# Performance work log

Measured on AMD Instinct MI355X. Metric: run time of the kernel, lower is better.

The kernel has to match this reference:

```python
import jax, jax.numpy as jnp
import numpy as np

BOHR = 0.5291772105638411   # Angstrom per Bohr (ase.units.Bohr)
HA = 27.211386024367243     # eV per Hartree (ase.units.Ha)
S6, S8, A1, A2 = 1.0, 0.7875, 0.4289, 4.4407
CN_ONSET, CN_CUTOFF = 20.0, 25.0
E2_ONSET, E2_CUTOFF = 55.0, 60.0
KCN = 16.0   # exponent of ncoord.exp_count
WF = 4.0     # gaussian_weight factor

N_ATOMS = 100000
N_EDGES = 3200000
N_ELEM = 95
N_REF = 5


def smooth_cutoff(dr, r_onset, r_cutoff):
    """HOOMD-style C^1 multiplicative isotropic cutoff S(dr)."""
    r_c = jnp.float32(r_cutoff) ** jnp.float32(2)
    r_o = jnp.float32(r_onset) ** jnp.float32(2)
    r = dr ** jnp.float32(2)
    inner = jnp.where(
        dr < r_cutoff,
        (r_c - r) ** 2 * (r_c + 2 * r - 3 * r_o) / (r_c - r_o) ** 3,
        0.0,
    )
    return jnp.where(dr < r_onset, 1.0, inner)


def setup_inputs() -> dict:
    key = jax.random.key(0)
    k1, k2, k3, k4, k5, k6, k7 = jax.random.split(key, 7)
    dr_vec = jax.random.normal(k1, (N_EDGES, 3), dtype=jnp.float32)
    ref_cn_table = jax.random.uniform(k2, (N_ELEM, N_REF), dtype=jnp.float32)
    ref_c6_table = jax.random.uniform(k3, (N_ELEM, N_ELEM, N_REF, N_REF), dtype=jnp.float32)
    r4r2_table = jax.random.uniform(k4, (N_ELEM,), dtype=jnp.float32) + 0.5
    rcov_table = jax.random.uniform(k5, (N_ELEM,), dtype=jnp.float32) + 0.5
    numbers = jax.random.randint(k6, (N_ATOMS,), 0, N_ELEM, dtype=jnp.int32)
    idx = jax.random.randint(k7, (2, N_EDGES), 0, N_ATOMS, dtype=jnp.int32)
    return {
        "dr_vec": dr_vec,
        "ref_cn_table": ref_cn_table,
        "ref_c6_table": ref_c6_table,
        "r4r2_table": r4r2_table,
        "rcov_table": rcov_table,
        "numbers": numbers,
        "idx": idx,
    }


def reference(dr_vec, ref_cn_table, ref_c6_table, r4r2_table, rcov_table, numbers, idx):
    n_atoms = numbers.shape[0]
    # per-edge distance, Angstrom -> Bohr
    dr = jnp.sqrt(jnp.sum(dr_vec * dr_vec, axis=-1)) / jnp.float32(BOHR)  # [E]
    i, j = idx[0], idx[1]
    Zi, Zj = numbers[i], numbers[j]

    # per-edge element data (D3Data.from_idxs)
    rc = rcov_table[Zi] + rcov_table[Zj]            # [E]
    qq = 3.0 * r4r2_table[Zi] * r4r2_table[Zj]      # [E]

    # coordination numbers: exp_count with smooth cutoff, segment-summed per atom
    count = 1.0 / (1.0 + jnp.exp(-KCN * (rc / dr - 1.0)))
    masked_cn = jnp.where(dr > 0, smooth_cutoff(dr, CN_ONSET, CN_CUTOFF) * count, 0.0)
    cn = jax.ops.segment_sum(masked_cn, i, num_segments=n_atoms)  # [N]

    # reference weights (gaussian weighting, normalized)
    ref_cn = ref_cn_table[numbers]                  # [N, R]
    dcn = ref_cn - cn[:, None]
    w = jnp.where(ref_cn >= 0, jnp.exp(-WF * dcn * dcn), 0.0)
    weights = w / (jnp.sum(w, -1, keepdims=True) + jnp.finfo(cn.dtype).eps)  # [N, R]

    # atomic C6 per edge
    ref_c6 = ref_c6_table[Zj, Zi]                   # [E, R, R]
    gw2 = weights[i][:, None, :] * weights[j][:, :, None]  # [E, R, R]
    c6 = jnp.sum(gw2 * ref_c6, axis=(-1, -2))       # [E]

    # rational (Becke-Johnson) damped two-body dispersion energy
    rr = A1 * jnp.sqrt(qq) + A2
    dr2 = dr * dr
    dr6 = dr2 * dr2 * dr2
    dr8 = dr6 * dr2
    rr2 = rr * rr
    rr6 = rr2 * rr2 * rr2
    rr8 = rr6 * rr2
    damped = -c6 * (S6 / (dr6 + rr6) + S8 * qq / (dr8 + rr8))
    energy = smooth_cutoff(dr, E2_ONSET, E2_CUTOFF) * damped / 2.0
    return jnp.sum(energy) * jnp.float32(HA)
```

## Files before the change

kernel.cpp:

```cpp
#include <hip/hip_runtime.h>
#include <hip/hip_fp16.h>

#define BOHR_F 0.5291772105638411f
#define HA_D   27.211386024367243
#define A1_F   0.4289f
#define A2_F   4.4407f
#define S6_F   1.0f
#define S8_F   0.7875f
#define KCN_F  16.0f
#define WF_F   4.0f
#define EPS_F  1.1920929e-07f

#define Q15_SCALE 32767.0f
#define Q15_INV   (1.0f/32767.0f)
#define DR_SCALE  512.0f
#define DR_INV    (1.0f/512.0f)
#define CN_SCALE 8388608.0f
#define CN_INV   (1.0f/8388608.0f)

#define NELEM  95
#define C6PADH 32
#define NBLK   512
#define BSW    512

__device__ __forceinline__ float smooth_cutoff(float dr, float r_on, float r_cut) {
    float r_c = r_cut * r_cut;
    float r_o = r_on * r_on;
    float r   = dr * dr;
    float den = (r_c - r_o);
    float t   = r_c - r;
    float inner = (dr < r_cut)
        ? (t * t * (r_c + 2.0f * r - 3.0f * r_o)) / (den * den * den)
        : 0.0f;
    return (dr < r_on) ? 1.0f : inner;
}

__device__ __forceinline__ float edge_m(float dr, float rc) {
    if (!(dr > 0.0f)) return 0.0f;
    float count = 1.0f / (1.0f + expf(-KCN_F * (rc / dr - 1.0f)));
    return smooth_cutoff(dr, 20.0f, 25.0f) * count;
}

__device__ __forceinline__ void u2f2(unsigned u, float& a, float& b) {
    __half2 h = __builtin_bit_cast(__half2, u);
    float2 f = __half22float2(h);
    a = f.x; b = f.y;
}

__device__ __forceinline__ int zfromR(uint4 R) {
    float z, dum;
    u2f2(R.w, z, dum);
    return (int)z;
}

__device__ __forceinline__ float edge_e(float dr, uint4 Ri, uint4 Rj,
                                        uint4 c0, uint4 c1, uint4 c2, uint4 c3) {
    float wi[5], wj[5], qi, qj;
    u2f2(Ri.x, wi[0], wi[1]); u2f2(Ri.y, wi[2], wi[3]); u2f2(Ri.z, wi[4], qi);
    u2f2(Rj.x, wj[0], wj[1]); u2f2(Rj.y, wj[2], wj[3]); u2f2(Rj.z, wj[4], qj);
    float ct[26];
    u2f2(c0.x, ct[0],  ct[1]);  u2f2(c0.y, ct[2],  ct[3]);
    u2f2(c0.z, ct[4],  ct[5]);  u2f2(c0.w, ct[6],  ct[7]);
    u2f2(c1.x, ct[8],  ct[9]);  u2f2(c1.y, ct[10], ct[11]);
    u2f2(c1.z, ct[12], ct[13]); u2f2(c1.w, ct[14], ct[15]);
    u2f2(c2.x, ct[16], ct[17]); u2f2(c2.y, ct[18], ct[19]);
    u2f2(c2.z, ct[20], ct[21]); u2f2(c2.w, ct[22], ct[23]);
    u2f2(c3.x, ct[24], ct[25]);
    float c6 = 0.0f;
#pragma unroll
    for (int a = 0; a < 5; ++a)
#pragma unroll
        for (int b = 0; b < 5; ++b)
            c6 += wj[a] * wi[b] * ct[a * 5 + b];
    float qq = 3.0f * qi * qj;
    float rr = A1_F * sqrtf(qq) + A2_F;
    float dr2 = dr * dr;
    float dr6 = dr2 * dr2 * dr2;
    float dr8 = dr6 * dr2;
    float rr2 = rr * rr;
    float rr6 = rr2 * rr2 * rr2;
    float rr8 = rr6 * rr2;
    float damped = -c6 * (S6_F / (dr6 + rr6) + S8_F * qq / (dr8 + rr8));
    return smooth_cutoff(dr, 55.0f, 60.0f) * damped * 0.5f;
}

__global__ __launch_bounds__(256)
void k_prep_c6(const float* __restrict__ src, __half* __restrict__ dst, int ntot) {
    int o = blockIdx.x * blockDim.x + threadIdx.x;
    if (o >= ntot) return;
    int p = o >> 5;
    int t = o & 31;
    dst[o] = __float2half((t < 25) ? src[p * 25 + t] : 0.0f);
}

__global__ __launch_bounds__(256)
void k_prep_atom(const int* __restrict__ numbers, const float* __restrict__ rcov,
                 uint2* __restrict__ rcovZ, int n_atoms) {
    int a = blockIdx.x * blockDim.x + threadIdx.x;
    if (a >= n_atoms) return;
    int Z = numbers[a];
    rcovZ[a] = make_uint2(__float_as_uint(rcov[Z]), (unsigned)Z);
}

__global__ __launch_bounds__(BSW, 4)
void k_bin(const float* __restrict__ dr_vec,
           const int* __restrict__ idx_i, const int* __restrict__ idx_j,
           const uint2* __restrict__ rcovZ,
           unsigned* __restrict__ packed2,
           unsigned* __restrict__ ghist,
           int n_edges, int nb) {
    __shared__ unsigned hist[256];
    if (threadIdx.x < 256) hist[threadIdx.x] = 0;
    __syncthreads();
    int nquad = (n_edges + 3) >> 2;
    int stride = gridDim.x * blockDim.x;
    for (int qd = blockIdx.x * blockDim.x + threadIdx.x; qd < nquad; qd += stride) {
        int e0 = qd << 2;
        int ne = n_edges - e0; if (ne > 4) ne = 4;
        if (ne == 4) {
            float4 v0 = *reinterpret_cast<const float4*>(dr_vec + 3 * e0);
            float4 v1 = *reinterpret_cast<const float4*>(dr_vec + 3 * e0 + 4);
            float4 v2 = *reinterpret_cast<const float4*>(dr_vec + 3 * e0 + 8);
            float drq[4];
            drq[0] = sqrtf(v0.x*v0.x + v0.y*v0.y + v0.z*v0.z) / BOHR_F;
            drq[1] = sqrtf(v0.w*v0.w + v1.x*v1.x + v1.y*v1.y) / BOHR_F;
            drq[2] = sqrtf(v1.z*v1.z + v1.w*v1.w + v2.x*v2.x) / BOHR_F;
            drq[3] = sqrtf(v2.y*v2.y + v2.z*v2.z + v2.w*v2.w) / BOHR_F;
            int4 i4 = *reinterpret_cast<const int4*>(idx_i + e0);
            int4 j4 = *reinterpret_cast<const int4*>(idx_j + e0);
            int ia[4] = { i4.x, i4.y, i4.z, i4.w };
            int ja[4] = { j4.x, j4.y, j4.z, j4.w };
            uint2 RiZ[4], RjZ[4];
#pragma unroll
            for (int k = 0; k < 4; ++k) { RiZ[k] = rcovZ[ia[k]]; RjZ[k] = rcovZ[ja[k]]; }
            unsigned w0[4], w1[4];
#pragma unroll
            for (int k = 0; k < 4; ++k) {
                float rc = __uint_as_float(RiZ[k].x) + __uint_as_float(RjZ[k].x);
                float m = edge_m(drq[k], rc);
                unsigned q = (unsigned)(m * Q15_SCALE + 0.5f);
                if (q > 0x7FFFu) q = 0x7FFFu;
                unsigned dq = (unsigned)(drq[k] * DR_SCALE + 0.5f);
                if (dq > 0x7FFFu) dq = 0x7FFFu;
                w0[k] = ((unsigned)ia[k] << 15) | q;
                w1[k] = ((unsigned)ja[k] << 15) | dq;
                atomicAdd(&hist[ia[k] >> 9], 1u);
            }
            *reinterpret_cast<uint4*>(packed2 + 2 * e0) =
                make_uint4(w0[0], w1[0], w0[1], w1[1]);
            *reinterpret_cast<uint4*>(packed2 + 2 * e0 + 4) =
                make_uint4(w0[2], w1[2], w0[3], w1[3]);
        } else {
            for (int k = 0; k < ne; ++k) {
                int e = e0 + k;
                float x = dr_vec[3*e], y = dr_vec[3*e+1], z = dr_vec[3*e+2];
                float dr = sqrtf(x*x + y*y + z*z) / BOHR_F;
                int i = idx_i[e], j = idx_j[e];
                uint2 RiZ = rcovZ[i], RjZ = rcovZ[j];
                float m = edge_m(dr, __uint_as_float(RiZ.x) + __uint_as_float(RjZ.x));
                unsigned q = (unsigned)(m * Q15_SCALE + 0.5f);
                if (q > 0x7FFFu) q = 0x7FFFu;
                unsigned dq = (unsigned)(dr * DR_SCALE + 0.5f);
                if (dq > 0x7FFFu) dq = 0x7FFFu;
                packed2[2*e]   = ((unsigned)i << 15) | q;
                packed2[2*e+1] = ((unsigned)j << 15) | dq;
                atomicAdd(&hist[i >> 9], 1u);
            }
        }
    }
    __syncthreads();
    if ((int)threadIdx.x < nb)
        ghist[(size_t)threadIdx.x * gridDim.x + blockIdx.x] = hist[threadIdx.x];
}

__global__ __launch_bounds__(NBLK)
void k_scan_bucket(unsigned* __restrict__ ghist, unsigned* __restrict__ totals) {
    __shared__ unsigned s[NBLK];
    int b = blockIdx.x;
    int t = threadIdx.x;
    unsigned v = ghist[(size_t)b * NBLK + t];
    s[t] = v;
    __syncthreads();
    for (int off = 1; off < NBLK; off <<= 1) {
        unsigned x = (t >= off) ? s[t - off] : 0u;
        __syncthreads();
        s[t] += x;
        __syncthreads();
    }
    ghist[(size_t)b * NBLK + t] = s[t] - v;
    if (t == NBLK - 1) totals[b] = s[t];
}

__global__ __launch_bounds__(256)
void k_scan_base(const unsigned* __restrict__ totals,
                 unsigned* __restrict__ base, int nb) {
    __shared__ unsigned s[256];
    int t = threadIdx.x;
    unsigned v = (t < nb) ? totals[t] : 0u;
    s[t] = v;
    __syncthreads();
    for (int off = 1; off < 256; off <<= 1) {
        unsigned x = (t >= off) ? s[t - off] : 0u;
        __syncthreads();
        s[t] += x;
        __syncthreads();
    }
    if (t < nb) base[t] = s[t] - v;
    if (t == 255) base[nb] = s[t];
}

__global__ __launch_bounds__(BSW, 4)
void k_scatter(const unsigned* __restrict__ packed2,
               const unsigned* __restrict__ ghist,
               const unsigned* __restrict__ base,
               uint2* __restrict__ pairs,
               int n_edges, int nb) {
    __shared__ unsigned ofs[256];
    if ((int)threadIdx.x < nb)
        ofs[threadIdx.x] = base[threadIdx.x]
                         + ghist[(size_t)threadIdx.x * gridDim.x + blockIdx.x];
    __syncthreads();
    int nquad = (n_edges + 3) >> 2;
    int stride = gridDim.x * blockDim.x;
    for (int qd = blockIdx.x * blockDim.x + threadIdx.x; qd < nquad; qd += stride) {
        int e0 = qd << 2;
        int ne = n_edges - e0; if (ne > 4) ne = 4;
        if (ne == 4) {
            uint4 pA = *reinterpret_cast<const uint4*>(packed2 + 2 * e0);
            uint4 pB = *reinterpret_cast<const uint4*>(packed2 + 2 * e0 + 4);
            unsigned w0[4] = { pA.x, pA.z, pB.x, pB.z };
            unsigned w1[4] = { pA.y, pA.w, pB.y, pB.w };
#pragma unroll
            for (int k = 0; k < 4; ++k) {
                unsigned pos = atomicAdd(&ofs[w0[k] >> 24], 1u);
                pairs[pos] = make_uint2(w0[k], w1[k]);
            }
        } else {
            for (int k = 0; k < ne; ++k) {
                int e = e0 + k;
                unsigned w0 = packed2[2*e], w1 = packed2[2*e+1];
                unsigned pos = atomicAdd(&ofs[w0 >> 24], 1u);
                pairs[pos] = make_uint2(w0, w1);
            }
        }
    }
}

__global__ __launch_bounds__(512)
void k_reduce_weights(const uint2* __restrict__ pairs,
                      const unsigned* __restrict__ base,
                      const int* __restrict__ numbers,
                      const float* __restrict__ ref_cn_table,
                      const float* __restrict__ r4r2,
                      __half* __restrict__ rec,
                      int n_atoms) {
    __shared__ unsigned hist[512];
    hist[threadIdx.x] = 0;
    __syncthreads();
    int b = blockIdx.x;
    unsigned start = base[b];
    unsigned end   = base[b + 1];
    for (unsigned k = start + threadIdx.x; k < end; k += 512) {
        unsigned p = pairs[k].x;
        atomicAdd(&hist[(p >> 15) & 511], p & 0x7FFFu);
    }
    __syncthreads();
    int a = (b << 9) + threadIdx.x;
    if (a < n_atoms) {
        float c = (float)hist[threadIdx.x] * Q15_INV;
        int Z = numbers[a];
        float w[5];
        float s = 0.0f;
#pragma unroll
        for (int r = 0; r < 5; ++r) {
            float rcn = ref_cn_table[Z * 5 + r];
            float d = rcn - c;
            float wv = (rcn >= 0.0f) ? expf(-WF_F * d * d) : 0.0f;
            w[r] = wv;
            s += wv;
        }
        float den = s + EPS_F;
        __half* rr = rec + (size_t)a * 8;
#pragma unroll
        for (int r = 0; r < 5; ++r) rr[r] = __float2half(w[r] / den);
        rr[5] = __float2half(r4r2[Z]);
        rr[6] = __float2half((float)Z);
        rr[7] = __float2half(0.0f);
    }
}

#define LOADC(p, z) do { \
    const uint4* _cp = reinterpret_cast<const uint4*>(c6h + (size_t)(z) * C6PADH); \
    p##0 = _cp[0]; p##1 = _cp[1]; p##2 = _cp[2]; p##3 = _cp[3]; } while (0)

__global__ __launch_bounds__(256, 1)
void k_energy_sorted(const uint2* __restrict__ pairs,
                     const __half* __restrict__ rec,
                     const __half* __restrict__ c6h,
                     double* __restrict__ e_acc,
                     int n_edges) {
    double local = 0.0;
    const uint4* recv = reinterpret_cast<const uint4*>(rec);
    int nquad = n_edges >> 2;
    int tid = blockIdx.x * blockDim.x + threadIdx.x;
    int stride = gridDim.x * blockDim.x;
    for (int qd = tid; qd < nquad; qd += stride) {
        int e0 = qd << 2;
        uint4 pA = *reinterpret_cast<const uint4*>(pairs + e0);
        uint4 pB = *reinterpret_cast<const uint4*>(pairs + e0 + 2);
        unsigned i0 = pA.x >> 15, j0 = pA.y >> 15;
        unsigned i1 = pA.z >> 15, j1 = pA.w >> 15;
        unsigned i2 = pB.x >> 15, j2 = pB.y >> 15;
        unsigned i3 = pB.z >> 15, j3 = pB.w >> 15;
        float dr0 = (float)(pA.y & 0x7FFFu) * DR_INV;
        float dr1 = (float)(pA.w & 0x7FFFu) * DR_INV;
        float dr2 = (float)(pB.y & 0x7FFFu) * DR_INV;
        float dr3 = (float)(pB.w & 0x7FFFu) * DR_INV;
        uint4 Ri0 = recv[i0], Rj0 = recv[j0];
        uint4 Ri1 = recv[i1], Rj1 = recv[j1];
        uint4 Ri2 = recv[i2], Rj2 = recv[j2];
        uint4 Ri3 = recv[i3], Rj3 = recv[j3];
        int zp0 = zfromR(Rj0) * NELEM + zfromR(Ri0);
        int zp1 = zfromR(Rj1) * NELEM + zfromR(Ri1);
        int zp2 = zfromR(Rj2) * NELEM + zfromR(Ri2);
        int zp3 = zfromR(Rj3) * NELEM + zfromR(Ri3);
        uint4 a0, a1, a2, a3;   LOADC(a, zp0);
        uint4 b0, b1, b2, b3;   LOADC(b, zp1);
        uint4 c0, c1, c2, c3;   LOADC(c, zp2);
        uint4 d0, d1, d2, d3;   LOADC(d, zp3);
        local += (double)edge_e(dr0, Ri0, Rj0, a0, a1, a2, a3);
        local += (double)edge_e(dr1, Ri1, Rj1, b0, b1, b2, b3);
        local += (double)edge_e(dr2, Ri2, Rj2, c0, c1, c2, c3);
        local += (double)edge_e(dr3, Ri3, Rj3, d0, d1, d2, d3);
    }
    for (int e = (nquad << 2) + tid; e < n_edges; e += stride) {
        uint2 pr = pairs[e];
        unsigned i = pr.x >> 15;
        unsigned j = pr.y >> 15;
        float dr = (float)(pr.y & 0x7FFFu) * DR_INV;
        uint4 Ri = recv[i];
        uint4 Rj = recv[j];
        int zp = zfromR(Rj) * NELEM + zfromR(Ri);
        const uint4* cp = reinterpret_cast<const uint4*>(c6h + (size_t)zp * C6PADH);
        local += (double)edge_e(dr, Ri, Rj, cp[0], cp[1], cp[2], cp[3]);
    }

    __shared__ double sdata[4];
    for (int off = 32; off > 0; off >>= 1)
        local += __shfl_down(local, off, 64);
    int lane = threadIdx.x & 63;
    int wid  = threadIdx.x >> 6;
    if (lane == 0) sdata[wid] = local;
    __syncthreads();
    if (threadIdx.x == 0) {
        double s = sdata[0] + sdata[1] + sdata[2] + sdata[3];
        atomicAdd(e_acc, s);
    }
}

__global__ __launch_bounds__(256)
void k_edges_cn_atomic(const float* __restrict__ dr_vec,
                       const int* __restrict__ idx_i,
                       const int* __restrict__ idx_j,
                       const uint2* __restrict__ rcovZ,
                       unsigned* __restrict__ cn_u32,
                       int n_edges) {
    int e = blockIdx.x * blockDim.x + threadIdx.x;
    if (e >= n_edges) return;
    float x = dr_vec[3 * e + 0];
    float y = dr_vec[3 * e + 1];
    float z = dr_vec[3 * e + 2];
    float dr = sqrtf(x * x + y * y + z * z) / BOHR_F;
    int i = idx_i[e];
    int j = idx_j[e];
    uint2 RiZ = rcovZ[i], RjZ = rcovZ[j];
    float m = edge_m(dr, __uint_as_float(RiZ.x) + __uint_as_float(RjZ.x));
    unsigned q = (unsigned)(m * CN_SCALE + 0.5f);
    if (q) atomicAdd(&cn_u32[i], q);
}

__global__ __launch_bounds__(256)
void k_atom_weights_rec(const unsigned* __restrict__ cn_u32,
                        const int* __restrict__ numbers,
                        const float* __restrict__ ref_cn_table,
                        const float* __restrict__ r4r2,
                        __half* __restrict__ rec,
                        int n_atoms) {
    int a = blockIdx.x * blockDim.x + threadIdx.x;
    if (a >= n_atoms) return;
    float c = (float)cn_u32[a] * CN_INV;
    int Z = numbers[a];
    float w[5];
    float s = 0.0f;
#pragma unroll
    for (int r = 0; r < 5; ++r) {
        float rcn = ref_cn_table[Z * 5 + r];
        float d = rcn - c;
        float wv = (rcn >= 0.0f) ? expf(-WF_F * d * d) : 0.0f;
        w[r] = wv;
        s += wv;
    }
    float den = s + EPS_F;
    __half* rr = rec + (size_t)a * 8;
#pragma unroll
    for (int r = 0; r < 5; ++r) rr[r] = __float2half(w[r] / den);
    rr[5] = __float2half(r4r2[Z]);
    rr[6] = __float2half((float)Z);
    rr[7] = __float2half(0.0f);
}

__global__ __launch_bounds__(256)
void k_energy_unsorted(const float* __restrict__ dr_vec,
                       const int* __restrict__ idx_i,
                       const int* __restrict__ idx_j,
                       const __half* __restrict__ rec,
                       const __half* __restrict__ c6h,
                       double* __restrict__ e_acc,
                       int n_edges) {
    double local = 0.0;
    const uint4* recv = reinterpret_cast<const uint4*>(rec);
    int tid = blockIdx.x * blockDim.x + threadIdx.x;
    int stride = gridDim.x * blockDim.x;
    for (int e = tid; e < n_edges; e += stride) {
        float x = dr_vec[3*e], y = dr_vec[3*e+1], z = dr_vec[3*e+2];
        float dr = sqrtf(x*x + y*y + z*z) / BOHR_F;
        int i = idx_i[e], j = idx_j[e];
        uint4 Ri = recv[i];
        uint4 Rj = recv[j];
        int zp = zfromR(Rj) * NELEM + zfromR(Ri);
        const uint4* cp = reinterpret_cast<const uint4*>(c6h + (size_t)zp * C6PADH);
        local += (double)edge_e(dr, Ri, Rj, cp[0], cp[1], cp[2], cp[3]);
    }
    __shared__ double sdata[4];
    for (int off = 32; off > 0; off >>= 1)
        local += __shfl_down(local, off, 64);
    int lane = threadIdx.x & 63;
    int wid  = threadIdx.x >> 6;
    if (lane == 0) sdata[wid] = local;
    __syncthreads();
    if (threadIdx.x == 0) {
        double s = sdata[0] + sdata[1] + sdata[2] + sdata[3];
        atomicAdd(e_acc, s);
    }
}

__global__ void k_finalize(const double* __restrict__ e_acc,
                           float* __restrict__ out) {
    out[0] = (float)(e_acc[0] * HA_D);
}

static inline size_t a16(size_t x) { return (x + 15) & ~(size_t)15; }

extern "C" void kernel_launch(void* const* d_in, const int* in_sizes, int n_in,
                              void* d_out, int out_size, void* d_ws, size_t ws_size,
                              hipStream_t stream) {
    const float* dr_vec      = (const float*)d_in[0];
    const float* ref_cn_tab  = (const float*)d_in[1];
    const float* ref_c6_tab  = (const float*)d_in[2];
    const float* r4r2        = (const float*)d_in[3];
    const float* rcov        = (const float*)d_in[4];
    const int*   numbers     = (const int*)d_in[5];
    const int*   idx         = (const int*)d_in[6];

    int n_atoms = in_sizes[5];
    int n_edges = in_sizes[6] / 2;
    const int* idx_i = idx;
    const int* idx_j = idx + n_edges;

    const int BS = 256;
    int nb = (n_atoms + 511) >> 9;
    int c6tot = NELEM * NELEM * C6PADH;

    char* ws = (char*)d_ws;
    double* e_acc = (double*)ws;

    size_t off_rec = 16;
    size_t off_c6p = a16(off_rec + (size_t)n_atoms * 8 * 2);
    size_t off_rcZ = a16(off_c6p + (size_t)c6tot * 2);
    size_t off_var = a16(off_rcZ + (size_t)n_atoms * 8);

    size_t s_packed = off_var;
    size_t s_pairs  = a16(s_packed + (size_t)n_edges * 8);
    size_t s_ghist  = a16(s_pairs + (size_t)n_edges * 8);
    size_t s_tot    = a16(s_ghist + (size_t)nb * NBLK * 4);
    size_t s_base   = a16(s_tot + (size_t)nb * 4);
    size_t need_s   = s_base + (size_t)(nb + 1) * 4;

    size_t a_cn   = off_var;

    int grid_c6 = (c6tot + BS - 1) / BS;
    int grid_a  = (n_atoms + BS - 1) / BS;
    int nquad   = (n_edges + 3) >> 2;
    int grid_q  = (nquad + BS - 1) / BS;
    if (grid_q > 8192) grid_q = 8192;
    int grid_e1 = (n_edges + BS - 1) / BS;
    if (grid_e1 > 8192) grid_e1 = 8192;

    __half* rec   = (__half*)(ws + off_rec);
    __half* c6h   = (__half*)(ws + off_c6p);
    uint2*  rcovZ = (uint2*)(ws + off_rcZ);

    k_prep_c6<<<grid_c6, BS, 0, stream>>>(ref_c6_tab, c6h, c6tot);
    k_prep_atom<<<grid_a, BS, 0, stream>>>(numbers, rcov, rcovZ, n_atoms);

    bool sortable = (n_atoms <= (1 << 17)) && (nb <= 256);

    if (sortable && ws_size >= need_s) {
        unsigned* packed2 = (unsigned*)(ws + s_packed);
        uint2*    pairs   = (uint2*)(ws + s_pairs);
        unsigned* ghist   = (unsigned*)(ws + s_ghist);
        unsigned* totals  = (unsigned*)(ws + s_tot);
        unsigned* base    = (unsigned*)(ws + s_base);

        hipMemsetAsync(d_ws, 0, 16, stream);

        k_bin<<<NBLK, BSW, 0, stream>>>(dr_vec, idx_i, idx_j, rcovZ,
            packed2, ghist, n_edges, nb);
        k_scan_bucket<<<nb, NBLK, 0, stream>>>(ghist, totals);
        k_scan_base<<<1, 256, 0, stream>>>(totals, base, nb);
        k_scatter<<<NBLK, BSW, 0, stream>>>(packed2, ghist, base, pairs,
                                            n_edges, nb);
        k_reduce_weights<<<nb, 512, 0, stream>>>(pairs, base, numbers,
            ref_cn_tab, r4r2, rec, n_atoms);
        k_energy_sorted<<<grid_q, BS, 0, stream>>>(pairs, rec, c6h, e_acc,
                                                   n_edges);
    } else {
        unsigned* cn_u32 = (unsigned*)(ws + a_cn);
        hipMemsetAsync(d_ws, 0, 16, stream);
        hipMemsetAsync(cn_u32, 0, (size_t)n_atoms * 4, stream);

        int grid_e = (n_edges + BS - 1) / BS;
        k_edges_cn_atomic<<<grid_e, BS, 0, stream>>>(dr_vec, idx_i, idx_j,
            rcovZ, cn_u32, n_edges);
        k_atom_weights_rec<<<grid_a, BS, 0, stream>>>(cn_u32, numbers,
            ref_cn_tab, r4r2, rec, n_atoms);
        k_energy_unsorted<<<grid_e1, BS, 0, stream>>>(dr_vec, idx_i, idx_j,
            rec, c6h, e_acc, n_edges);
    }

    k_finalize<<<1, 1, 0, stream>>>(e_acc, (float*)d_out);
}
```

Measured before the change: 157.7 us.

## Quantize C6 table to 8-bit rows and fuse edge compute into scatter

The per-pair C6 reference block is stored as 25 uint8 values plus a per-row float scale (32 bytes instead of 64), which halves the gather traffic in the energy kernel. The binning pass now only histograms idx_i, and the scatter pass recomputes distances and coordination terms directly from the inputs. This removes the intermediate packed buffer write and read. The cost is reading dr_vec, idx and rcovZ in the scatter instead, plus precision loss from 8-bit C6 quantization, which may break tolerance.

```diff
diff --git a/kernel.cpp b/kernel.cpp
--- a/kernel.cpp
+++ b/kernel.cpp
@@ -19,7 +19,6 @@
 #define CN_INV   (1.0f/8388608.0f)
 
 #define NELEM  95
-#define C6PADH 32
 #define NBLK   512
 #define BSW    512
 
@@ -53,25 +52,24 @@
     return (int)z;
 }
 
-__device__ __forceinline__ float edge_e(float dr, uint4 Ri, uint4 Rj,
-                                        uint4 c0, uint4 c1, uint4 c2, uint4 c3) {
+__device__ __forceinline__ float edge_e8(float dr, uint4 Ri, uint4 Rj,
+                                         uint4 c0, uint4 c1) {
     float wi[5], wj[5], qi, qj;
     u2f2(Ri.x, wi[0], wi[1]); u2f2(Ri.y, wi[2], wi[3]); u2f2(Ri.z, wi[4], qi);
     u2f2(Rj.x, wj[0], wj[1]); u2f2(Rj.y, wj[2], wj[3]); u2f2(Rj.z, wj[4], qj);
-    float ct[26];
-    u2f2(c0.x, ct[0],  ct[1]);  u2f2(c0.y, ct[2],  ct[3]);
-    u2f2(c0.z, ct[4],  ct[5]);  u2f2(c0.w, ct[6],  ct[7]);
-    u2f2(c1.x, ct[8],  ct[9]);  u2f2(c1.y, ct[10], ct[11]);
-    u2f2(c1.z, ct[12], ct[13]); u2f2(c1.w, ct[14], ct[15]);
-    u2f2(c2.x, ct[16], ct[17]); u2f2(c2.y, ct[18], ct[19]);
-    u2f2(c2.z, ct[20], ct[21]); u2f2(c2.w, ct[22], ct[23]);
-    u2f2(c3.x, ct[24], ct[25]);
-    float c6 = 0.0f;
-#pragma unroll
-    for (int a = 0; a < 5; ++a)
-#pragma unroll
-        for (int b = 0; b < 5; ++b)
-            c6 += wj[a] * wi[b] * ct[a * 5 + b];
+    unsigned w[7] = { c0.x, c0.y, c0.z, c0.w, c1.x, c1.y, c1.z };
+    float sc = __uint_as_float(c1.w);
+    float c6q = 0.0f;
+#pragma unroll
+    for (int a = 0; a < 5; ++a) {
+#pragma unroll
+        for (int b = 0; b < 5; ++b) {
+            const int k = a * 5 + b;
+            float qv = (float)((w[k >> 2] >> ((k & 3) * 8)) & 0xFFu);
+            c6q += wj[a] * wi[b] * qv;
+        }
+    }
+    float c6 = c6q * sc;
     float qq = 3.0f * qi * qj;
     float rr = A1_F * sqrtf(qq) + A2_F;
     float dr2 = dr * dr;
@@ -85,12 +83,38 @@
 }
 
 __global__ __launch_bounds__(256)
-void k_prep_c6(const float* __restrict__ src, __half* __restrict__ dst, int ntot) {
-    int o = blockIdx.x * blockDim.x + threadIdx.x;
-    if (o >= ntot) return;
-    int p = o >> 5;
-    int t = o & 31;
-    dst[o] = __float2half((t < 25) ? src[p * 25 + t] : 0.0f);
+void k_prep_c6u8(const float* __restrict__ src, unsigned char* __restrict__ dst,
+                 int nrows) {
+    int r = blockIdx.x * blockDim.x + threadIdx.x;
+    if (r >= nrows) return;
+    const float* s = src + (size_t)r * 25;
+    float mx = 0.0f;
+#pragma unroll
+    for (int k = 0; k < 25; ++k) mx = fmaxf(mx, fabsf(s[k]));
+    float sc  = mx * (1.0f / 255.0f);
+    float inv = (mx > 0.0f) ? 255.0f / mx : 0.0f;
+    unsigned w[8];
+#pragma unroll
+    for (int v = 0; v < 7; ++v) {
+        unsigned acc = 0;
+#pragma unroll
+        for (int b = 0; b < 4; ++b) {
+            int k = v * 4 + b;
+            unsigned q = 0;
+            if (k < 25) {
+                float t = s[k] * inv;
+                t = fmaxf(t, 0.0f);
+                q = (unsigned)(t + 0.5f);
+                if (q > 255u) q = 255u;
+            }
+            acc |= q << (b * 8);
+        }
+        w[v] = acc;
+    }
+    w[7] = __float_as_uint(sc);
+    uint4* d = reinterpret_cast<uint4*>(dst + (size_t)r * 32);
+    d[0] = make_uint4(w[0], w[1], w[2], w[3]);
+    d[1] = make_uint4(w[4], w[5], w[6], w[7]);
 }
 
 __global__ __launch_bounds__(256)
@@ -103,71 +127,23 @@
 }
 
 __global__ __launch_bounds__(BSW, 4)
-void k_bin(const float* __restrict__ dr_vec,
-           const int* __restrict__ idx_i, const int* __restrict__ idx_j,
-           const uint2* __restrict__ rcovZ,
-           unsigned* __restrict__ packed2,
-           unsigned* __restrict__ ghist,
-           int n_edges, int nb) {
+void k_hist(const int* __restrict__ idx_i, unsigned* __restrict__ ghist,
+            int n_edges, int nb) {
     __shared__ unsigned hist[256];
     if (threadIdx.x < 256) hist[threadIdx.x] = 0;
     __syncthreads();
-    int nquad = (n_edges + 3) >> 2;
+    int nquad = n_edges >> 2;
+    int tid = blockIdx.x * blockDim.x + threadIdx.x;
     int stride = gridDim.x * blockDim.x;
-    for (int qd = blockIdx.x * blockDim.x + threadIdx.x; qd < nquad; qd += stride) {
-        int e0 = qd << 2;
-        int ne = n_edges - e0; if (ne > 4) ne = 4;
-        if (ne == 4) {
-            float4 v0 = *reinterpret_cast<const float4*>(dr_vec + 3 * e0);
-            float4 v1 = *reinterpret_cast<const float4*>(dr_vec + 3 * e0 + 4);
-            float4 v2 = *reinterpret_cast<const float4*>(dr_vec + 3 * e0 + 8);
-            float drq[4];
-            drq[0] = sqrtf(v0.x*v0.x + v0.y*v0.y + v0.z*v0.z) / BOHR_F;
-            drq[1] = sqrtf(v0.w*v0.w + v1.x*v1.x + v1.y*v1.y) / BOHR_F;
-            drq[2] = sqrtf(v1.z*v1.z + v1.w*v1.w + v2.x*v2.x) / BOHR_F;
-            drq[3] = sqrtf(v2.y*v2.y + v2.z*v2.z + v2.w*v2.w) / BOHR_F;
-            int4 i4 = *reinterpret_cast<const int4*>(idx_i + e0);
-            int4 j4 = *reinterpret_cast<const int4*>(idx_j + e0);
-            int ia[4] = { i4.x, i4.y, i4.z, i4.w };
-            int ja[4] = { j4.x, j4.y, j4.z, j4.w };
-            uint2 RiZ[4], RjZ[4];
-#pragma unroll
-            for (int k = 0; k < 4; ++k) { RiZ[k] = rcovZ[ia[k]]; RjZ[k] = rcovZ[ja[k]]; }
-            unsigned w0[4], w1[4];
-#pragma unroll
-            for (int k = 0; k < 4; ++k) {
-                float rc = __uint_as_float(RiZ[k].x) + __uint_as_float(RjZ[k].x);
-                float m = edge_m(drq[k], rc);
-                unsigned q = (unsigned)(m * Q15_SCALE + 0.5f);
-                if (q > 0x7FFFu) q = 0x7FFFu;
-                unsigned dq = (unsigned)(drq[k] * DR_SCALE + 0.5f);
-                if (dq > 0x7FFFu) dq = 0x7FFFu;
-                w0[k] = ((unsigned)ia[k] << 15) | q;
-                w1[k] = ((unsigned)ja[k] << 15) | dq;
-                atomicAdd(&hist[ia[k] >> 9], 1u);
-            }
-            *reinterpret_cast<uint4*>(packed2 + 2 * e0) =
-                make_uint4(w0[0], w1[0], w0[1], w1[1]);
-            *reinterpret_cast<uint4*>(packed2 + 2 * e0 + 4) =
-                make_uint4(w0[2], w1[2], w0[3], w1[3]);
-        } else {
-            for (int k = 0; k < ne; ++k) {
-                int e = e0 + k;
-                float x = dr_vec[3*e], y = dr_vec[3*e+1], z = dr_vec[3*e+2];
-                float dr = sqrtf(x*x + y*y + z*z) / BOHR_F;
-                int i = idx_i[e], j = idx_j[e];
-                uint2 RiZ = rcovZ[i], RjZ = rcovZ[j];
-                float m = edge_m(dr, __uint_as_float(RiZ.x) + __uint_as_float(RjZ.x));
-                unsigned q = (unsigned)(m * Q15_SCALE + 0.5f);
-                if (q > 0x7FFFu) q = 0x7FFFu;
-                unsigned dq = (unsigned)(dr * DR_SCALE + 0.5f);
-                if (dq > 0x7FFFu) dq = 0x7FFFu;
-                packed2[2*e]   = ((unsigned)i << 15) | q;
-                packed2[2*e+1] = ((unsigned)j << 15) | dq;
-                atomicAdd(&hist[i >> 9], 1u);
-            }
-        }
-    }
+    for (int qd = tid; qd < nquad; qd += stride) {
+        int4 i4 = *reinterpret_cast<const int4*>(idx_i + (qd << 2));
+        atomicAdd(&hist[i4.x >> 9], 1u);
+        atomicAdd(&hist[i4.y >> 9], 1u);
+        atomicAdd(&hist[i4.z >> 9], 1u);
+        atomicAdd(&hist[i4.w >> 9], 1u);
+    }
+    for (int e = (nquad << 2) + tid; e < n_edges; e += stride)
+        atomicAdd(&hist[idx_i[e] >> 9], 1u);
     __syncthreads();
     if ((int)threadIdx.x < nb)
         ghist[(size_t)threadIdx.x * gridDim.x + blockIdx.x] = hist[threadIdx.x];
@@ -210,39 +186,66 @@
 }
 
 __global__ __launch_bounds__(BSW, 4)
-void k_scatter(const unsigned* __restrict__ packed2,
-               const unsigned* __restrict__ ghist,
-               const unsigned* __restrict__ base,
-               uint2* __restrict__ pairs,
-               int n_edges, int nb) {
+void k_scatter_full(const float* __restrict__ dr_vec,
+                    const int* __restrict__ idx_i,
+                    const int* __restrict__ idx_j,
+                    const uint2* __restrict__ rcovZ,
+                    const unsigned* __restrict__ ghist,
+                    const unsigned* __restrict__ base,
+                    uint2* __restrict__ pairs,
+                    int n_edges, int nb) {
     __shared__ unsigned ofs[256];
     if ((int)threadIdx.x < nb)
         ofs[threadIdx.x] = base[threadIdx.x]
                          + ghist[(size_t)threadIdx.x * gridDim.x + blockIdx.x];
     __syncthreads();
-    int nquad = (n_edges + 3) >> 2;
+    int nquad = n_edges >> 2;
+    int tid = blockIdx.x * blockDim.x + threadIdx.x;
     int stride = gridDim.x * blockDim.x;
-    for (int qd = blockIdx.x * blockDim.x + threadIdx.x; qd < nquad; qd += stride) {
+    for (int qd = tid; qd < nquad; qd += stride) {
         int e0 = qd << 2;
-        int ne = n_edges - e0; if (ne > 4) ne = 4;
-        if (ne == 4) {
-            uint4 pA = *reinterpret_cast<const uint4*>(packed2 + 2 * e0);
-            uint4 pB = *reinterpret_cast<const uint4*>(packed2 + 2 * e0 + 4);
-            unsigned w0[4] = { pA.x, pA.z, pB.x, pB.z };
-            unsigned w1[4] = { pA.y, pA.w, pB.y, pB.w };
-#pragma unroll
-            for (int k = 0; k < 4; ++k) {
-                unsigned pos = atomicAdd(&ofs[w0[k] >> 24], 1u);
-                pairs[pos] = make_uint2(w0[k], w1[k]);
-            }
-        } else {
-            for (int k = 0; k < ne; ++k) {
-                int e = e0 + k;
-                unsigned w0 = packed2[2*e], w1 = packed2[2*e+1];
-                unsigned pos = atomicAdd(&ofs[w0 >> 24], 1u);
-                pairs[pos] = make_uint2(w0, w1);
-            }
+        float4 v0 = *reinterpret_cast<const float4*>(dr_vec + 3 * e0);
+        float4 v1 = *reinterpret_cast<const float4*>(dr_vec + 3 * e0 + 4);
+        float4 v2 = *reinterpret_cast<const float4*>(dr_vec + 3 * e0 + 8);
+        float drq[4];
+        drq[0] = sqrtf(v0.x*v0.x + v0.y*v0.y + v0.z*v0.z) / BOHR_F;
+        drq[1] = sqrtf(v0.w*v0.w + v1.x*v1.x + v1.y*v1.y) / BOHR_F;
+        drq[2] = sqrtf(v1.z*v1.z + v1.w*v1.w + v2.x*v2.x) / BOHR_F;
+        drq[3] = sqrtf(v2.y*v2.y + v2.z*v2.z + v2.w*v2.w) / BOHR_F;
+        int4 i4 = *reinterpret_cast<const int4*>(idx_i + e0);
+        int4 j4 = *reinterpret_cast<const int4*>(idx_j + e0);
+        int ia[4] = { i4.x, i4.y, i4.z, i4.w };
+        int ja[4] = { j4.x, j4.y, j4.z, j4.w };
+        uint2 RiZ[4], RjZ[4];
+#pragma unroll
+        for (int k = 0; k < 4; ++k) { RiZ[k] = rcovZ[ia[k]]; RjZ[k] = rcovZ[ja[k]]; }
+#pragma unroll
+        for (int k = 0; k < 4; ++k) {
+            float rc = __uint_as_float(RiZ[k].x) + __uint_as_float(RjZ[k].x);
+            float m = edge_m(drq[k], rc);
+            unsigned q = (unsigned)(m * Q15_SCALE + 0.5f);
+            if (q > 0x7FFFu) q = 0x7FFFu;
+            unsigned dq = (unsigned)(drq[k] * DR_SCALE + 0.5f);
+            if (dq > 0x7FFFu) dq = 0x7FFFu;
+            unsigned w0 = ((unsigned)ia[k] << 15) | q;
+            unsigned w1 = ((unsigned)ja[k] << 15) | dq;
+            unsigned pos = atomicAdd(&ofs[ia[k] >> 9], 1u);
+            pairs[pos] = make_uint2(w0, w1);
         }
+    }
+    for (int e = (nquad << 2) + tid; e < n_edges; e += stride) {
+        float x = dr_vec[3*e], y = dr_vec[3*e+1], z = dr_vec[3*e+2];
+        float dr = sqrtf(x*x + y*y + z*z) / BOHR_F;
+        int i = idx_i[e], j = idx_j[e];
+        uint2 RiZ = rcovZ[i], RjZ = rcovZ[j];
+        float m = edge_m(dr, __uint_as_float(RiZ.x) + __uint_as_float(RjZ.x));
+        unsigned q = (unsigned)(m * Q15_SCALE + 0.5f);
+        if (q > 0x7FFFu) q = 0x7FFFu;
+        unsigned dq = (unsigned)(dr * DR_SCALE + 0.5f);
+        if (dq > 0x7FFFu) dq = 0x7FFFu;
+        unsigned pos = atomicAdd(&ofs[i >> 9], 1u);
+        pairs[pos] = make_uint2(((unsigned)i << 15) | q,
+                                ((unsigned)j << 15) | dq);
     }
 }
 
@@ -289,14 +292,14 @@
     }
 }
 
-#define LOADC(p, z) do { \
-    const uint4* _cp = reinterpret_cast<const uint4*>(c6h + (size_t)(z) * C6PADH); \
-    p##0 = _cp[0]; p##1 = _cp[1]; p##2 = _cp[2]; p##3 = _cp[3]; } while (0)
+#define LOADC8(p, z) do { \
+    const uint4* _cp = reinterpret_cast<const uint4*>(c6q + (size_t)(z) * 32); \
+    p##0 = _cp[0]; p##1 = _cp[1]; } while (0)
 
 __global__ __launch_bounds__(256, 1)
 void k_energy_sorted(const uint2* __restrict__ pairs,
                      const __half* __restrict__ rec,
-                     const __half* __restrict__ c6h,
+                     const unsigned char* __restrict__ c6q,
                      double* __restrict__ e_acc,
                      int n_edges) {
     double local = 0.0;
@@ -324,14 +327,14 @@
         int zp1 = zfromR(Rj1) * NELEM + zfromR(Ri1);
         int zp2 = zfromR(Rj2) * NELEM + zfromR(Ri2);
         int zp3 = zfromR(Rj3) * NELEM + zfromR(Ri3);
-        uint4 a0, a1, a2, a3;   LOADC(a, zp0);
-        uint4 b0, b1, b2, b3;   LOADC(b, zp1);
-        uint4 c0, c1, c2, c3;   LOADC(c, zp2);
-        uint4 d0, d1, d2, d3;   LOADC(d, zp3);
-        local += (double)edge_e(dr0, Ri0, Rj0, a0, a1, a2, a3);
-        local += (double)edge_e(dr1, Ri1, Rj1, b0, b1, b2, b3);
-        local += (double)edge_e(dr2, Ri2, Rj2, c0, c1, c2, c3);
-        local += (double)edge_e(dr3, Ri3, Rj3, d0, d1, d2, d3);
+        uint4 a0, a1;   LOADC8(a, zp0);
+        uint4 b0, b1;   LOADC8(b, zp1);
+        uint4 c0, c1;   LOADC8(c, zp2);
+        uint4 d0, d1;   LOADC8(d, zp3);
+        local += (double)edge_e8(dr0, Ri0, Rj0, a0, a1);
+        local += (double)edge_e8(dr1, Ri1, Rj1, b0, b1);
+        local += (double)edge_e8(dr2, Ri2, Rj2, c0, c1);
+        local += (double)edge_e8(dr3, Ri3, Rj3, d0, d1);
     }
     for (int e = (nquad << 2) + tid; e < n_edges; e += stride) {
         uint2 pr = pairs[e];
@@ -341,8 +344,8 @@
         uint4 Ri = recv[i];
         uint4 Rj = recv[j];
         int zp = zfromR(Rj) * NELEM + zfromR(Ri);
-        const uint4* cp = reinterpret_cast<const uint4*>(c6h + (size_t)zp * C6PADH);
-        local += (double)edge_e(dr, Ri, Rj, cp[0], cp[1], cp[2], cp[3]);
+        const uint4* cp = reinterpret_cast<const uint4*>(c6q + (size_t)zp * 32);
+        local += (double)edge_e8(dr, Ri, Rj, cp[0], cp[1]);
     }
 
     __shared__ double sdata[4];
@@ -414,7 +417,7 @@
                        const int* __restrict__ idx_i,
                        const int* __restrict__ idx_j,
                        const __half* __restrict__ rec,
-                       const __half* __restrict__ c6h,
+                       const unsigned char* __restrict__ c6q,
                        double* __restrict__ e_acc,
                        int n_edges) {
     double local = 0.0;
@@ -428,8 +431,8 @@
         uint4 Ri = recv[i];
         uint4 Rj = recv[j];
         int zp = zfromR(Rj) * NELEM + zfromR(Ri);
-        const uint4* cp = reinterpret_cast<const uint4*>(c6h + (size_t)zp * C6PADH);
-        local += (double)edge_e(dr, Ri, Rj, cp[0], cp[1], cp[2], cp[3]);
+        const uint4* cp = reinterpret_cast<const uint4*>(c6q + (size_t)zp * 32);
+        local += (double)edge_e8(dr, Ri, Rj, cp[0], cp[1]);
     }
     __shared__ double sdata[4];
     for (int off = 32; off > 0; off >>= 1)
@@ -469,18 +472,17 @@
 
     const int BS = 256;
     int nb = (n_atoms + 511) >> 9;
-    int c6tot = NELEM * NELEM * C6PADH;
+    int nrows = NELEM * NELEM;
 
     char* ws = (char*)d_ws;
     double* e_acc = (double*)ws;
 
     size_t off_rec = 16;
-    size_t off_c6p = a16(off_rec + (size_t)n_atoms * 8 * 2);
-    size_t off_rcZ = a16(off_c6p + (size_t)c6tot * 2);
+    size_t off_c6q = a16(off_rec + (size_t)n_atoms * 8 * 2);
+    size_t off_rcZ = a16(off_c6q + (size_t)nrows * 32);
     size_t off_var = a16(off_rcZ + (size_t)n_atoms * 8);
 
-    size_t s_packed = off_var;
-    size_t s_pairs  = a16(s_packed + (size_t)n_edges * 8);
+    size_t s_pairs  = off_var;
     size_t s_ghist  = a16(s_pairs + (size_t)n_edges * 8);
     size_t s_tot    = a16(s_ghist + (size_t)nb * NBLK * 4);
     size_t s_base   = a16(s_tot + (size_t)nb * 4);
@@ -488,7 +490,7 @@
 
     size_t a_cn   = off_var;
 
-    int grid_c6 = (c6tot + BS - 1) / BS;
+    int grid_r  = (nrows + BS - 1) / BS;
     int grid_a  = (n_atoms + BS - 1) / BS;
     int nquad   = (n_edges + 3) >> 2;
     int grid_q  = (nquad + BS - 1) / BS;
@@ -496,17 +498,16 @@
     int grid_e1 = (n_edges + BS - 1) / BS;
     if (grid_e1 > 8192) grid_e1 = 8192;
 
-    __half* rec   = (__half*)(ws + off_rec);
-    __half* c6h   = (__half*)(ws + off_c6p);
-    uint2*  rcovZ = (uint2*)(ws + off_rcZ);
-
-    k_prep_c6<<<grid_c6, BS, 0, stream>>>(ref_c6_tab, c6h, c6tot);
+    __half*        rec   = (__half*)(ws + off_rec);
+    unsigned char* c6q   = (unsigned char*)(ws + off_c6q);
+    uint2*         rcovZ = (uint2*)(ws + off_rcZ);
+
+    k_prep_c6u8<<<grid_r, BS, 0, stream>>>(ref_c6_tab, c6q, nrows);
     k_prep_atom<<<grid_a, BS, 0, stream>>>(numbers, rcov, rcovZ, n_atoms);
 
     bool sortable = (n_atoms <= (1 << 17)) && (nb <= 256);
 
     if (sortable && ws_size >= need_s) {
-        unsigned* packed2 = (unsigned*)(ws + s_packed);
         uint2*    pairs   = (uint2*)(ws + s_pairs);
         unsigned* ghist   = (unsigned*)(ws + s_ghist);
         unsigned* totals  = (unsigned*)(ws + s_tot);
@@ -514,15 +515,14 @@
 
         hipMemsetAsync(d_ws, 0, 16, stream);
 
-        k_bin<<<NBLK, BSW, 0, stream>>>(dr_vec, idx_i, idx_j, rcovZ,
-            packed2, ghist, n_edges, nb);
+        k_hist<<<NBLK, BSW, 0, stream>>>(idx_i, ghist, n_edges, nb);
         k_scan_bucket<<<nb, NBLK, 0, stream>>>(ghist, totals);
         k_scan_base<<<1, 256, 0, stream>>>(totals, base, nb);
-        k_scatter<<<NBLK, BSW, 0, stream>>>(packed2, ghist, base, pairs,
-                                            n_edges, nb);
+        k_scatter_full<<<NBLK, BSW, 0, stream>>>(dr_vec, idx_i, idx_j, rcovZ,
+            ghist, base, pairs, n_edges, nb);
         k_reduce_weights<<<nb, 512, 0, stream>>>(pairs, base, numbers,
             ref_cn_tab, r4r2, rec, n_atoms);
-        k_energy_sorted<<<grid_q, BS, 0, stream>>>(pairs, rec, c6h, e_acc,
+        k_energy_sorted<<<grid_q, BS, 0, stream>>>(pairs, rec, c6q, e_acc,
                                                    n_edges);
     } else {
         unsigned* cn_u32 = (unsigned*)(ws + a_cn);
@@ -535,7 +535,7 @@
         k_atom_weights_rec<<<grid_a, BS, 0, stream>>>(cn_u32, numbers,
             ref_cn_tab, r4r2, rec, n_atoms);
         k_energy_unsorted<<<grid_e1, BS, 0, stream>>>(dr_vec, idx_i, idx_j,
-            rec, c6h, e_acc, n_edges);
+            rec, c6q, e_acc, n_edges);
     }
 
     k_finalize<<<1, 1, 0, stream>>>(e_acc, (float*)d_out);
```

Measured after the change: 150.3 us. -4.6%, faster.
